# Performance work log

Measured on AMD Instinct MI355X. Metric: run time of the kernel, lower is better.

The kernel has to match this reference:

```python
import jax, jax.numpy as jnp
import numpy as np

H = 1024  # hidden_size


def _lstm_layer(x, w_ih, w_hh, b_ih, b_hh):
    # x: [S, B, I] -> outputs [S, B, H]
    S, B, _ = x.shape
    # Precompute input projection for all timesteps (both biases folded in,
    # matching gi + gh where gi carries b_ih and gh carries b_hh).
    gi = jnp.einsum('sbi,gi->sbg', x, w_ih) + b_ih + b_hh  # [S, B, 4H]
    h0 = jnp.zeros((B, H), x.dtype)
    c0 = jnp.zeros((B, H), x.dtype)

    def step(carry, gi_t):
        h, c = carry
        gates = gi_t + h @ w_hh.T                # [B, 4H]
        i, f, g, o = jnp.split(gates, 4, axis=1)  # gate order: i, f, g, o
        c_new = jax.nn.sigmoid(f) * c + jax.nn.sigmoid(i) * jnp.tanh(g)
        h_new = jax.nn.sigmoid(o) * jnp.tanh(c_new)
        return (h_new, c_new), h_new

    (h_last, c_last), ys = jax.lax.scan(step, (h0, c0), gi)
    return ys, h_last, c_last


def setup_inputs() -> dict:
    key = jax.random.key(0)
    ks = jax.random.split(key, 6)
    S, B, I = 512, 64, 1024
    def xavier(k, shape):
        fan_out, fan_in = shape
        lim = np.sqrt(6.0 / (fan_in + fan_out)).astype(np.float32)
        return jax.random.uniform(k, shape, jnp.float32, -lim, lim)
    return {
        'x': jax.random.normal(ks[0], (S, B, I), jnp.float32),
        'w_ih_0': xavier(ks[1], (4 * H, I)),
        'w_hh_0': xavier(ks[2], (4 * H, H)),
        'b_ih_0': jnp.zeros((4 * H,), jnp.float32),
        'b_hh_0': jnp.zeros((4 * H,), jnp.float32),
        'w_ih_1': xavier(ks[3], (4 * H, H)),
        'w_hh_1': xavier(ks[4], (4 * H, H)),
        'b_ih_1': jnp.zeros((4 * H,), jnp.float32),
        'b_hh_1': jnp.zeros((4 * H,), jnp.float32),
    }


def reference(x, w_ih_0, w_hh_0, b_ih_0, b_hh_0, w_ih_1, w_hh_1, b_ih_1, b_hh_1):
    # 2-layer unidirectional LSTM, dropout=0, batch_first=False, zero init state.
    y0, h0, c0 = _lstm_layer(x, w_ih_0, w_hh_0, b_ih_0, b_hh_0)
    y1, h1, c1 = _lstm_layer(y0, w_ih_1, w_hh_1, b_ih_1, b_hh_1)
    h_n = jnp.stack([h0, h1], axis=0)  # [num_layers, B, H]
    c_n = jnp.stack([c0, c1], axis=0)
    return y1, h_n, c_n
```

## Files before the change

### kernel.cpp

```cpp
#include <hip/hip_runtime.h>

typedef __attribute__((ext_vector_type(8))) short short8;
typedef __attribute__((ext_vector_type(4))) float f32x4;
typedef unsigned int uint32;
typedef unsigned long long u64;

#define OFF_GI    0ull
#define OFF_XB    268435456ull
#define OFF_WIH0  335544320ull
#define OFF_WIH1  343932928ull
#define OFF_WPK0  352321536ull
#define OFF_WPK1  360710144ull
#define OFF_B0    369098752ull
#define OFF_B1    369115136ull
#define OFF_CNT   369131520ull
#define OFF_HBUF  369164288ull
#define WS_REQUIRED 369426432ull

__device__ __forceinline__ unsigned short f2bf(float f) {
    union { float f; uint32 u; } v; v.f = f;
    uint32 u = v.u + 0x7FFFu + ((v.u >> 16) & 1u);
    return (unsigned short)(u >> 16);
}
__device__ __forceinline__ float bf2f(unsigned short u) {
    union { uint32 u; float f; } v; v.u = ((uint32)u) << 16; return v.f;
}
__device__ __forceinline__ float sigmoidf_(float x) {
    return 1.0f / (1.0f + __expf(-x));
}
__device__ __forceinline__ float tanhf_(float x) {
    return 1.0f - 2.0f / (1.0f + __expf(2.0f * x));
}

__global__ void diag_kernel(float* out, float val) {
    if (blockIdx.x == 0 && threadIdx.x == 0) out[0] = val;
}

__global__ void cast_bf16_kernel(const float* __restrict__ in,
                                 unsigned short* __restrict__ out, int n4) {
    int i = blockIdx.x * 256 + threadIdx.x;
    if (i < n4) {
        float4 v = ((const float4*)in)[i];
        ushort4 o;
        o.x = f2bf(v.x); o.y = f2bf(v.y); o.z = f2bf(v.z); o.w = f2bf(v.w);
        ((ushort4*)out)[i] = o;
    }
}

__global__ void bias_sum_kernel(const float* __restrict__ a,
                                const float* __restrict__ b,
                                float* __restrict__ o, int n) {
    int i = blockIdx.x * 256 + threadIdx.x;
    if (i < n) o[i] = a[i] + b[i];
}

__global__ void pack_whh_kernel(const float* __restrict__ whh,
                                unsigned short* __restrict__ out) {
    int o = blockIdx.x * 256 + threadIdx.x;
    int j  = o & 7;
    int l  = (o >> 3) & 63;
    int f  = (o >> 9) & 31;
    int wq = o >> 14;
    int w = wq >> 2, q = wq & 3;
    int g = f >> 3,  s = f & 7;
    int n = g * 1024 + w * 16 + (l & 15);
    int k = q * 256 + s * 32 + ((l >> 4)) * 8 + j;
    out[o] = f2bf(whh[(size_t)n * 1024 + k]);
}

__global__ __launch_bounds__(256, 2) void gemm_bt_kernel(
    const unsigned short* __restrict__ A,
    const unsigned short* __restrict__ B,
    const float* __restrict__ bias,
    unsigned short* __restrict__ C) {
    __shared__ __align__(16) unsigned short As[128 * 64];
    __shared__ __align__(16) unsigned short Bs[128 * 64];
    const int tid = threadIdx.x;
    const int l = tid & 63;
    const int wv = tid >> 6;
    const int wm = wv >> 1, wn = wv & 1;
    const long bm = blockIdx.x, bn = blockIdx.y;

    f32x4 acc[4][4];
#pragma unroll
    for (int i = 0; i < 4; ++i)
#pragma unroll
        for (int j = 0; j < 4; ++j)
            acc[i][j] = (f32x4){0.f, 0.f, 0.f, 0.f};

    for (int k0 = 0; k0 < 1024; k0 += 64) {
#pragma unroll
        for (int ii = 0; ii < 4; ++ii) {
            int slot = ii * 256 + tid;
            int row = slot >> 3, csw = slot & 7;
            int cc = csw ^ (row & 7);
            *(uint4*)&As[slot * 8] =
                *(const uint4*)(A + (bm * 128 + row) * 1024 + k0 + cc * 8);
            *(uint4*)&Bs[slot * 8] =
                *(const uint4*)(B + (bn * 128 + row) * 1024 + k0 + cc * 8);
        }
        __syncthreads();
#pragma unroll
        for (int s = 0; s < 2; ++s) {
            short8 af[4], bfm[4];
#pragma unroll
            for (int i = 0; i < 4; ++i) {
                int row = wm * 64 + i * 16 + (l & 15);
                af[i] = *(const short8*)&As[(row * 8 + (((s * 4) + (l >> 4)) ^ (row & 7))) * 8];
            }
#pragma unroll
            for (int j = 0; j < 4; ++j) {
                int row = wn * 64 + j * 16 + (l & 15);
                bfm[j] = *(const short8*)&Bs[(row * 8 + (((s * 4) + (l >> 4)) ^ (row & 7))) * 8];
            }
#pragma unroll
            for (int i = 0; i < 4; ++i)
#pragma unroll
                for (int j = 0; j < 4; ++j)
                    acc[i][j] = __builtin_amdgcn_mfma_f32_16x16x32_bf16(
                        af[i], bfm[j], acc[i][j], 0, 0, 0);
        }
        __syncthreads();
    }
#pragma unroll
    for (int j = 0; j < 4; ++j) {
        float bj = bias[bn * 128 + wn * 64 + j * 16 + (l & 15)];
#pragma unroll
        for (int i = 0; i < 4; ++i) {
#pragma unroll
            for (int r = 0; r < 4; ++r) {
                long row = bm * 128 + wm * 64 + i * 16 + (l >> 4) * 4 + r;
                C[row * 4096 + bn * 128 + wn * 64 + j * 16 + (l & 15)] =
                    f2bf(acc[i][j][r] + bj);
            }
        }
    }
}

__global__ __launch_bounds__(256, 2) void lstm_rec_kernel(
    const unsigned short* __restrict__ gi,
    const unsigned short* __restrict__ wpk,
    unsigned short* hbuf,
    unsigned short* __restrict__ yb,
    float* __restrict__ yf,
    float* __restrict__ hn, float* __restrict__ cn,
    int* cnt) {
    __shared__ __align__(16) unsigned short hs[16 * 1024];
    __shared__ float red[4][4][16][16];
    const int tid = threadIdx.x;
    const int l = tid & 63, q = tid >> 6;
    const int W = blockIdx.x;
    const int p = W >> 6, w = W & 63;
    int* cg = cnt + p * 2048;

    short8 bfr[4][8];
    {
        const unsigned short* wb = wpk + (size_t)((w * 4 + q) * 32) * 512 + (size_t)l * 8;
#pragma unroll
        for (int g = 0; g < 4; ++g)
#pragma unroll
            for (int s = 0; s < 8; ++s)
                bfr[g][s] = *(const short8*)(wb + (g * 8 + s) * 512);
    }

    float c_state = 0.0f;
    const int be = tid >> 4, je = tid & 15;
    const int hrow = p * 16 + be;
    const int hcol = w * 16 + je;
    const size_t gi_base = (size_t)hrow * 4096 + hcol;

    for (int t = 0; t < 512; ++t) {
        const unsigned short* gp = gi + (size_t)t * 262144 + gi_base;
        float g0 = bf2f(gp[0]);
        float g1 = bf2f(gp[1024]);
        float g2 = bf2f(gp[2048]);
        float g3 = bf2f(gp[3072]);

        if (t > 0 && tid == 0) {
            int iters = 0;
            while (__hip_atomic_load(&cg[t - 1], __ATOMIC_RELAXED,
                                     __HIP_MEMORY_SCOPE_AGENT) < 64) {
                __builtin_amdgcn_s_sleep(2);
                if (++iters > 100000) break;
            }
        }
        __syncthreads();

        {
            const u64* hp64 = (const u64*)(hbuf + (size_t)(t & 1) * 65536);
#pragma unroll
            for (int ii = 0; ii < 8; ++ii) {
                int slot = ii * 256 + tid;
                int row = slot >> 7, cs = slot & 127;
                int cc = cs ^ (row & 7);
                size_t gidx = ((size_t)(p * 16 + row) * 1024 + (size_t)cc * 8) >> 2;
                u64 lo = __hip_atomic_load(&hp64[gidx], __ATOMIC_RELAXED,
                                           __HIP_MEMORY_SCOPE_AGENT);
                u64 hi = __hip_atomic_load(&hp64[gidx + 1], __ATOMIC_RELAXED,
                                           __HIP_MEMORY_SCOPE_AGENT);
                *(u64*)&hs[slot * 8]     = lo;
                *(u64*)&hs[slot * 8 + 4] = hi;
            }
        }
        __syncthreads();

        f32x4 acc[4];
#pragma unroll
        for (int g = 0; g < 4; ++g) acc[g] = (f32x4){0.f, 0.f, 0.f, 0.f};
        const int arow = l & 15;
#pragma unroll
        for (int s = 0; s < 8; ++s) {
            int chunk = q * 32 + s * 4 + (l >> 4);
            short8 af = *(const short8*)&hs[(arow * 128 + (chunk ^ (arow & 7))) * 8];
#pragma unroll
            for (int g = 0; g < 4; ++g)
                acc[g] = __builtin_amdgcn_mfma_f32_16x16x32_bf16(
                    af, bfr[g][s], acc[g], 0, 0, 0);
        }
#pragma unroll
        for (int g = 0; g < 4; ++g)
#pragma unroll
            for (int r = 0; r < 4; ++r)
                red[q][g][(l >> 4) * 4 + r][l & 15] = acc[g][r];
        __syncthreads();

        float gate_i = g0, gate_f = g1, gate_g = g2, gate_o = g3;
#pragma unroll
        for (int qq = 0; qq < 4; ++qq) {
            gate_i += red[qq][0][be][je];
            gate_f += red[qq][1][be][je];
            gate_g += red[qq][2][be][je];
            gate_o += red[qq][3][be][je];
        }
        float ig = sigmoidf_(gate_i);
        float fg = sigmoidf_(gate_f);
        float gg = tanhf_(gate_g);
        float og = sigmoidf_(gate_o);
        c_state = fg * c_state + ig * gg;
        float h_new = og * tanhf_(c_state);

        unsigned short hb = f2bf(h_new);
        {
            int v0 = hb;
            int v1 = __shfl_down(v0, 1);
            int v2 = __shfl_down(v0, 2);
            int v3 = __shfl_down(v0, 3);
            if ((l & 3) == 0) {
                u64 u = (u64)(v0 & 0xffff) | ((u64)(v1 & 0xffff) << 16) |
                        ((u64)(v2 & 0xffff) << 32) | ((u64)(v3 & 0xffff) << 48);
                u64* dst = (u64*)(hbuf + (size_t)((t + 1) & 1) * 65536 +
                                  (size_t)hrow * 1024 + hcol);
                __hip_atomic_store(dst, u, __ATOMIC_RELAXED,
                                   __HIP_MEMORY_SCOPE_AGENT);
            }
        }
        if (yb) yb[(size_t)t * 65536 + (size_t)hrow * 1024 + hcol] = hb;
        if (yf) yf[(size_t)t * 65536 + (size_t)hrow * 1024 + hcol] = h_new;
        if (t == 511) {
            hn[(size_t)hrow * 1024 + hcol] = h_new;
            cn[(size_t)hrow * 1024 + hcol] = c_state;
        }
        __syncthreads();
        if (tid == 0)
            __hip_atomic_fetch_add(&cg[t], 1, __ATOMIC_RELAXED,
                                   __HIP_MEMORY_SCOPE_AGENT);
    }
}

extern "C" void kernel_launch(void* const* d_in, const int* in_sizes, int n_in,
                              void* d_out, int out_size, void* d_ws, size_t ws_size,
                              hipStream_t stream) {
    const float* x    = (const float*)d_in[0];
    const float* wih0 = (const float*)d_in[1];
    const float* whh0 = (const float*)d_in[2];
    const float* bih0 = (const float*)d_in[3];
    const float* bhh0 = (const float*)d_in[4];
    const float* wih1 = (const float*)d_in[5];
    const float* whh1 = (const float*)d_in[6];
    const float* bih1 = (const float*)d_in[7];
    const float* bhh1 = (const float*)d_in[8];
    float* out = (float*)d_out;

    if (ws_size < WS_REQUIRED) {
        diag_kernel<<<1, 64, 0, stream>>>(out, (float)(ws_size >> 20));
        return;
    }

    char* ws = (char*)d_ws;
    unsigned short* gi    = (unsigned short*)(ws + OFF_GI);
    unsigned short* xb    = (unsigned short*)(ws + OFF_XB);
    unsigned short* y0b   = (unsigned short*)(ws + OFF_XB);
    unsigned short* wih0b = (unsigned short*)(ws + OFF_WIH0);
    unsigned short* wih1b = (unsigned short*)(ws + OFF_WIH1);
    unsigned short* wpk0  = (unsigned short*)(ws + OFF_WPK0);
    unsigned short* wpk1  = (unsigned short*)(ws + OFF_WPK1);
    float*          b0    = (float*)(ws + OFF_B0);
    float*          b1    = (float*)(ws + OFF_B1);
    int*            cnt   = (int*)(ws + OFF_CNT);
    unsigned short* hbuf  = (unsigned short*)(ws + OFF_HBUF);

    cast_bf16_kernel<<<32768, 256, 0, stream>>>(x, xb, 8388608);
    cast_bf16_kernel<<<4096, 256, 0, stream>>>(wih0, wih0b, 1048576);
    cast_bf16_kernel<<<4096, 256, 0, stream>>>(wih1, wih1b, 1048576);
    pack_whh_kernel<<<16384, 256, 0, stream>>>(whh0, wpk0);
    pack_whh_kernel<<<16384, 256, 0, stream>>>(whh1, wpk1);
    bias_sum_kernel<<<16, 256, 0, stream>>>(bih0, bhh0, b0, 4096);
    bias_sum_kernel<<<16, 256, 0, stream>>>(bih1, bhh1, b1, 4096);

    gemm_bt_kernel<<<dim3(256, 32), 256, 0, stream>>>(xb, wih0b, b0, gi);
    hipMemsetAsync(cnt, 0, 32768 + 262144, stream);
    lstm_rec_kernel<<<256, 256, 0, stream>>>(gi, wpk0, hbuf, y0b, nullptr,
                                             out + 33554432, out + 33685504, cnt);
    gemm_bt_kernel<<<dim3(256, 32), 256, 0, stream>>>(y0b, wih1b, b1, gi);
    hipMemsetAsync(cnt, 0, 32768 + 262144, stream);
    lstm_rec_kernel<<<256, 256, 0, stream>>>(gi, wpk1, hbuf, nullptr, out,
                                             out + 33554432 + 65536,
                                             out + 33685504 + 65536, cnt);
}
```

Baseline: 5.823 ms.

## Fuse layer-1 input projection into layer-0 recurrent kernel per timestep

At step t, each layer-0 block already holds h_{t-1} in shared memory. It now uses that tile to compute the layer-1 input-projection slice for t-1 with MFMA, using a fragment-packed W_ih1 and a gate-interleaved bias, and writes the result in place into the consumed gi rows. This removes the separate layer-1 GEMM launch and the bf16 y0 write/read round trip. The cost is extra MFMA work and weight-fragment loads from global memory inside the serial recurrent loop. That work runs after the step counter is signalled, so it is meant to overlap other blocks' waits. The spin watchdog limit is also lowered.

Measured after the change: 5.674 ms. 2.6% less time.

```diff
diff --git a/kernel.cpp b/kernel.cpp
--- a/kernel.cpp
+++ b/kernel.cpp
@@ -8,7 +8,7 @@
 #define OFF_GI    0ull
 #define OFF_XB    268435456ull
 #define OFF_WIH0  335544320ull
-#define OFF_WIH1  343932928ull
+#define OFF_WPKI  343932928ull
 #define OFF_WPK0  352321536ull
 #define OFF_WPK1  360710144ull
 #define OFF_B0    369098752ull
@@ -16,6 +16,11 @@
 #define OFF_CNT   369131520ull
 #define OFF_HBUF  369164288ull
 #define WS_REQUIRED 369426432ull
+
+#define ALOAD(p)    __hip_atomic_load((p), __ATOMIC_RELAXED, __HIP_MEMORY_SCOPE_AGENT)
+#define ASTOREV(p,v) __hip_atomic_store((p), (v), __ATOMIC_RELAXED, __HIP_MEMORY_SCOPE_AGENT)
+#define AADD(p,v)   __hip_atomic_fetch_add((p), (v), __ATOMIC_RELAXED, __HIP_MEMORY_SCOPE_AGENT)
+#define WD_ITERS 30000
 
 __device__ __forceinline__ unsigned short f2bf(float f) {
     union { float f; uint32 u; } v; v.f = f;
@@ -52,6 +57,14 @@
                                 float* __restrict__ o, int n) {
     int i = blockIdx.x * 256 + threadIdx.x;
     if (i < n) o[i] = a[i] + b[i];
+}
+
+__global__ void bias_perm_kernel(const float* __restrict__ a,
+                                 const float* __restrict__ b,
+                                 float* __restrict__ o) {
+    int i = blockIdx.x * 256 + threadIdx.x;
+    int c = i >> 2, g = i & 3;
+    o[i] = a[g * 1024 + c] + b[g * 1024 + c];
 }
 
 __global__ void pack_whh_kernel(const float* __restrict__ whh,
@@ -68,6 +81,20 @@
     out[o] = f2bf(whh[(size_t)n * 1024 + k]);
 }
 
+__global__ void pack_wih1_frag_kernel(const float* __restrict__ wih1,
+                                      unsigned short* __restrict__ out) {
+    int o = blockIdx.x * 256 + threadIdx.x;
+    int j  = o & 7;
+    int l  = (o >> 3) & 63;
+    int ks = (o >> 9) & 31;
+    int wq = o >> 14;
+    int w = wq >> 2, q = wq & 3;
+    int np = w * 64 + q * 16 + (l & 15);
+    int c = np >> 2, g = np & 3;
+    int k = ks * 32 + ((l >> 4)) * 8 + j;
+    out[o] = f2bf(wih1[(size_t)(g * 1024 + c) * 1024 + k]);
+}
+
 __global__ __launch_bounds__(256, 2) void gemm_bt_kernel(
     const unsigned short* __restrict__ A,
     const unsigned short* __restrict__ B,
@@ -137,11 +164,46 @@
     }
 }
 
+__device__ __forceinline__ void gi1_tile(
+    const unsigned short* hs,
+    const unsigned short* __restrict__ wpkI,
+    const float* __restrict__ b1p,
+    unsigned short* gi1,
+    int tg, int p, int w, int q, int l)
+{
+    f32x4 gacc = (f32x4){0.f, 0.f, 0.f, 0.f};
+    const int arow = l & 15;
+    const unsigned short* wb = wpkI + (size_t)(w * 4 + q) * 16384 + (size_t)l * 8;
+#pragma unroll 4
+    for (int ks = 0; ks < 32; ++ks) {
+        short8 bfk = *(const short8*)(wb + ks * 512);
+        short8 afk = *(const short8*)&hs[(arow * 128 + ((ks * 4 + (l >> 4)) ^ (arow & 7))) * 8];
+        gacc = __builtin_amdgcn_mfma_f32_16x16x32_bf16(afk, bfk, gacc, 0, 0, 0);
+    }
+    const int colp = w * 64 + q * 16 + (l & 15);
+    float bj = b1p[colp];
+#pragma unroll
+    for (int r = 0; r < 4; ++r) {
+        int v0 = f2bf(gacc[r] + bj);
+        int v1 = __shfl_down(v0, 1);
+        int v2 = __shfl_down(v0, 2);
+        int v3 = __shfl_down(v0, 3);
+        if ((l & 3) == 0) {
+            size_t row = (size_t)tg * 64 + p * 16 + (l >> 4) * 4 + r;
+            u64 u = (u64)(v0 & 0xffff) | ((u64)(v1 & 0xffff) << 16) |
+                    ((u64)(v2 & 0xffff) << 32) | ((u64)(v3 & 0xffff) << 48);
+            *(u64*)(gi1 + row * 4096 + colp) = u;
+        }
+    }
+}
+
+template <int LAYER>
 __global__ __launch_bounds__(256, 2) void lstm_rec_kernel(
-    const unsigned short* __restrict__ gi,
+    unsigned short* gi,
     const unsigned short* __restrict__ wpk,
+    const unsigned short* __restrict__ wpkI,
+    const float* __restrict__ b1p,
     unsigned short* hbuf,
-    unsigned short* __restrict__ yb,
     float* __restrict__ yf,
     float* __restrict__ hn, float* __restrict__ cn,
     int* cnt) {
@@ -167,21 +229,28 @@
     const int be = tid >> 4, je = tid & 15;
     const int hrow = p * 16 + be;
     const int hcol = w * 16 + je;
-    const size_t gi_base = (size_t)hrow * 4096 + hcol;
 
     for (int t = 0; t < 512; ++t) {
-        const unsigned short* gp = gi + (size_t)t * 262144 + gi_base;
-        float g0 = bf2f(gp[0]);
-        float g1 = bf2f(gp[1024]);
-        float g2 = bf2f(gp[2048]);
-        float g3 = bf2f(gp[3072]);
+        float g0, g1, g2, g3;
+        if (LAYER == 0) {
+            const unsigned short* gp = gi + (size_t)t * 262144 + (size_t)hrow * 4096 + hcol;
+            g0 = bf2f(gp[0]);
+            g1 = bf2f(gp[1024]);
+            g2 = bf2f(gp[2048]);
+            g3 = bf2f(gp[3072]);
+        } else {
+            u64 gv = *(const u64*)(gi + ((size_t)t * 64 + hrow) * 4096 + (size_t)hcol * 4);
+            g0 = bf2f((unsigned short)gv);
+            g1 = bf2f((unsigned short)(gv >> 16));
+            g2 = bf2f((unsigned short)(gv >> 32));
+            g3 = bf2f((unsigned short)(gv >> 48));
+        }
 
         if (t > 0 && tid == 0) {
             int iters = 0;
-            while (__hip_atomic_load(&cg[t - 1], __ATOMIC_RELAXED,
-                                     __HIP_MEMORY_SCOPE_AGENT) < 64) {
+            while (ALOAD(&cg[t - 1]) < 64) {
                 __builtin_amdgcn_s_sleep(2);
-                if (++iters > 100000) break;
+                if (++iters > WD_ITERS) break;
             }
         }
         __syncthreads();
@@ -194,10 +263,8 @@
                 int row = slot >> 7, cs = slot & 127;
                 int cc = cs ^ (row & 7);
                 size_t gidx = ((size_t)(p * 16 + row) * 1024 + (size_t)cc * 8) >> 2;
-                u64 lo = __hip_atomic_load(&hp64[gidx], __ATOMIC_RELAXED,
-                                           __HIP_MEMORY_SCOPE_AGENT);
-                u64 hi = __hip_atomic_load(&hp64[gidx + 1], __ATOMIC_RELAXED,
-                                           __HIP_MEMORY_SCOPE_AGENT);
+                u64 lo = ALOAD(&hp64[gidx]);
+                u64 hi = ALOAD(&hp64[gidx + 1]);
                 *(u64*)&hs[slot * 8]     = lo;
                 *(u64*)&hs[slot * 8 + 4] = hi;
             }
@@ -250,20 +317,47 @@
                         ((u64)(v2 & 0xffff) << 32) | ((u64)(v3 & 0xffff) << 48);
                 u64* dst = (u64*)(hbuf + (size_t)((t + 1) & 1) * 65536 +
                                   (size_t)hrow * 1024 + hcol);
-                __hip_atomic_store(dst, u, __ATOMIC_RELAXED,
-                                   __HIP_MEMORY_SCOPE_AGENT);
-            }
-        }
-        if (yb) yb[(size_t)t * 65536 + (size_t)hrow * 1024 + hcol] = hb;
+                ASTOREV(dst, u);
+            }
+        }
         if (yf) yf[(size_t)t * 65536 + (size_t)hrow * 1024 + hcol] = h_new;
         if (t == 511) {
             hn[(size_t)hrow * 1024 + hcol] = h_new;
             cn[(size_t)hrow * 1024 + hcol] = c_state;
         }
         __syncthreads();
-        if (tid == 0)
-            __hip_atomic_fetch_add(&cg[t], 1, __ATOMIC_RELAXED,
-                                   __HIP_MEMORY_SCOPE_AGENT);
+        if (tid == 0) AADD(&cg[t], 1);
+
+        if (LAYER == 0 && t > 0) {
+            gi1_tile(hs, wpkI, b1p, gi, t - 1, p, w, q, l);
+        }
+    }
+
+    if (LAYER == 0) {
+        if (tid == 0) {
+            int iters = 0;
+            while (ALOAD(&cg[511]) < 64) {
+                __builtin_amdgcn_s_sleep(2);
+                if (++iters > WD_ITERS) break;
+            }
+        }
+        __syncthreads();
+        {
+            const u64* hp64 = (const u64*)hbuf;
+#pragma unroll
+            for (int ii = 0; ii < 8; ++ii) {
+                int slot = ii * 256 + tid;
+                int row = slot >> 7, cs = slot & 127;
+                int cc = cs ^ (row & 7);
+                size_t gidx = ((size_t)(p * 16 + row) * 1024 + (size_t)cc * 8) >> 2;
+                u64 lo = ALOAD(&hp64[gidx]);
+                u64 hi = ALOAD(&hp64[gidx + 1]);
+                *(u64*)&hs[slot * 8]     = lo;
+                *(u64*)&hs[slot * 8 + 4] = hi;
+            }
+        }
+        __syncthreads();
+        gi1_tile(hs, wpkI, b1p, gi, 511, p, w, q, l);
     }
 }
 
@@ -289,31 +383,34 @@
     char* ws = (char*)d_ws;
     unsigned short* gi    = (unsigned short*)(ws + OFF_GI);
     unsigned short* xb    = (unsigned short*)(ws + OFF_XB);
-    unsigned short* y0b   = (unsigned short*)(ws + OFF_XB);
     unsigned short* wih0b = (unsigned short*)(ws + OFF_WIH0);
-    unsigned short* wih1b = (unsigned short*)(ws + OFF_WIH1);
+    unsigned short* wpkI  = (unsigned short*)(ws + OFF_WPKI);
     unsigned short* wpk0  = (unsigned short*)(ws + OFF_WPK0);
     unsigned short* wpk1  = (unsigned short*)(ws + OFF_WPK1);
     float*          b0    = (float*)(ws + OFF_B0);
-    float*          b1    = (float*)(ws + OFF_B1);
+    float*          b1p   = (float*)(ws + OFF_B1);
     int*            cnt   = (int*)(ws + OFF_CNT);
     unsigned short* hbuf  = (unsigned short*)(ws + OFF_HBUF);
 
     cast_bf16_kernel<<<32768, 256, 0, stream>>>(x, xb, 8388608);
     cast_bf16_kernel<<<4096, 256, 0, stream>>>(wih0, wih0b, 1048576);
-    cast_bf16_kernel<<<4096, 256, 0, stream>>>(wih1, wih1b, 1048576);
+    pack_wih1_frag_kernel<<<16384, 256, 0, stream>>>(wih1, wpkI);
     pack_whh_kernel<<<16384, 256, 0, stream>>>(whh0, wpk0);
     pack_whh_kernel<<<16384, 256, 0, stream>>>(whh1, wpk1);
     bias_sum_kernel<<<16, 256, 0, stream>>>(bih0, bhh0, b0, 4096);
-    bias_sum_kernel<<<16, 256, 0, stream>>>(bih1, bhh1, b1, 4096);
+    bias_perm_kernel<<<16, 256, 0, stream>>>(bih1, bhh1, b1p);
 
     gemm_bt_kernel<<<dim3(256, 32), 256, 0, stream>>>(xb, wih0b, b0, gi);
+
     hipMemsetAsync(cnt, 0, 32768 + 262144, stream);
-    lstm_rec_kernel<<<256, 256, 0, stream>>>(gi, wpk0, hbuf, y0b, nullptr,
-                                             out + 33554432, out + 33685504, cnt);
-    gemm_bt_kernel<<<dim3(256, 32), 256, 0, stream>>>(y0b, wih1b, b1, gi);
+    lstm_rec_kernel<0><<<256, 256, 0, stream>>>(gi, wpk0, wpkI, b1p, hbuf,
+                                                nullptr,
+                                                out + 33554432, out + 33685504,
+                                                cnt);
     hipMemsetAsync(cnt, 0, 32768 + 262144, stream);
-    lstm_rec_kernel<<<256, 256, 0, stream>>>(gi, wpk1, hbuf, nullptr, out,
-                                             out + 33554432 + 65536,
-                                             out + 33685504 + 65536, cnt);
-}
+    lstm_rec_kernel<1><<<256, 256, 0, stream>>>(gi, wpk1, wpkI, b1p, hbuf,
+                                                out,
+                                                out + 33554432 + 65536,
+                                                out + 33685504 + 65536,
+                                                cnt);
+}
```
